# Kernel tuning notes

Measured on AMD Instinct MI355X. Metric: run time of the kernel, lower is better.

## Reference

```python
import jax, jax.numpy as jnp
import numpy as np
from jax.ops import segment_sum

N_NODES = 100000
N_EDGES = 1600000
D = 128
N_LAYERS = 4
N_GRAPHS = 512
LN_EPS = 1e-5


def setup_inputs() -> dict:
    key = jax.random.key(0)
    ks = jax.random.split(key, 8)
    x = jax.random.normal(ks[0], (N_NODES, D), dtype=jnp.float32)
    edge_index = jax.random.randint(ks[1], (2, N_EDGES), 0, N_NODES, dtype=jnp.int64)
    batch = jnp.sort(jax.random.randint(ks[2], (N_NODES,), 0, N_GRAPHS, dtype=jnp.int64))
    scale = 1.0 / np.sqrt(D)
    Ws = jax.random.normal(ks[3], (N_LAYERS, D, D), dtype=jnp.float32) * scale
    bs = jnp.zeros((N_LAYERS, D), dtype=jnp.float32)
    gammas = jnp.ones((N_LAYERS, D), dtype=jnp.float32)
    betas = jnp.zeros((N_LAYERS, D), dtype=jnp.float32)
    lin_w = jax.random.normal(ks[4], (D, 1), dtype=jnp.float32) * scale
    lin_b = jnp.zeros((1,), dtype=jnp.float32)
    return {"x": x, "edge_index": edge_index, "batch": batch, "Ws": Ws,
            "bs": bs, "gammas": gammas, "betas": betas,
            "lin_w": lin_w, "lin_b": lin_b}


def _gcn_conv(x, W, b, src, dst, deg_inv_sqrt):
    # PyG GCNConv: h = x @ W, then sym-normalized aggregation over A + I, then + bias
    h = x @ W                                   # [N, D]
    coef = deg_inv_sqrt[src] * deg_inv_sqrt[dst]  # [E]
    msg = h[src] * coef[:, None]                # [E, D] gather (memory-bound)
    agg = segment_sum(msg, dst, num_segments=x.shape[0])  # scatter-add
    agg = agg + h * (deg_inv_sqrt * deg_inv_sqrt)[:, None]  # self-loop term
    return agg + b


def _layernorm(x, gamma, beta):
    mu = jnp.mean(x, axis=-1, keepdims=True)
    var = jnp.mean(jnp.square(x - mu), axis=-1, keepdims=True)
    return (x - mu) * jax.lax.rsqrt(var + LN_EPS) * gamma + beta


def reference(x, edge_index, batch, Ws, bs, gammas, betas, lin_w, lin_b):
    n = x.shape[0]
    src, dst = edge_index[0], edge_index[1]
    # degree with self-loops (GCNConv adds self loops by default)
    deg = segment_sum(jnp.ones_like(dst, dtype=x.dtype), dst, num_segments=n) + 1.0
    deg_inv_sqrt = jax.lax.rsqrt(deg)

    h = _gcn_conv(x, Ws[0], bs[0], src, dst, deg_inv_sqrt)
    h = _layernorm(h, gammas[0], betas[0])
    h = jax.nn.relu(h)  # dropout is identity in eval mode
    for i in range(1, N_LAYERS):
        h_prev = h
        h = _gcn_conv(h, Ws[i], bs[i], src, dst, deg_inv_sqrt)
        h = _layernorm(h, gammas[i], betas[i])
        h = h + h_prev
        if i < N_LAYERS - 1:
            h = jax.nn.relu(h)

    # global mean pool over graphs
    sums = segment_sum(h, batch, num_segments=N_GRAPHS)        # [G, D]
    cnts = segment_sum(jnp.ones((n,), h.dtype), batch, num_segments=N_GRAPHS)
    pooled = sums / jnp.maximum(cnts, 1.0)[:, None]
    return pooled @ lin_w + lin_b  # [G, 1]
```

## Files before the change

kernel.cpp:

```cpp
#include <hip/hip_runtime.h>
#include <hip/hip_bf16.h>


typedef __hip_bfloat162 bf2;
typedef __attribute__((ext_vector_type(8))) short short8;
typedef __attribute__((ext_vector_type(4))) float f32x4;

__global__ __launch_bounds__(256) void k_deg(const int* __restrict__ dst,
                                             int* __restrict__ cnt, int E) {
    int base = (blockIdx.x * 256 + threadIdx.x) * 4;
    if (base + 4 <= E) {
        int4 d4 = *(const int4*)(dst + base);
        atomicAdd(&cnt[d4.x], 1);
        atomicAdd(&cnt[d4.y], 1);
        atomicAdd(&cnt[d4.z], 1);
        atomicAdd(&cnt[d4.w], 1);
    } else {
        for (int j = base; j < E; j++) atomicAdd(&cnt[dst[j]], 1);
    }
}

__global__ __launch_bounds__(256) void k_scan1(const int* __restrict__ cnt,
                                               int* __restrict__ loc,
                                               int* __restrict__ blk,
                                               float* __restrict__ dis, int n) {
    __shared__ int s[256];
    int b = blockIdx.x, tid = threadIdx.x;
    int base = b * 1024 + tid * 4;
    int v0 = (base + 0 < n) ? cnt[base + 0] : 0;
    int v1 = (base + 1 < n) ? cnt[base + 1] : 0;
    int v2 = (base + 2 < n) ? cnt[base + 2] : 0;
    int v3 = (base + 3 < n) ? cnt[base + 3] : 0;
    if (base + 0 < n) dis[base + 0] = rsqrtf((float)v0 + 1.0f);
    if (base + 1 < n) dis[base + 1] = rsqrtf((float)v1 + 1.0f);
    if (base + 2 < n) dis[base + 2] = rsqrtf((float)v2 + 1.0f);
    if (base + 3 < n) dis[base + 3] = rsqrtf((float)v3 + 1.0f);
    int tsum = v0 + v1 + v2 + v3;
    s[tid] = tsum;
    __syncthreads();
    for (int off = 1; off < 256; off <<= 1) {
        int t = (tid >= off) ? s[tid - off] : 0;
        __syncthreads();
        s[tid] += t;
        __syncthreads();
    }
    int excl = s[tid] - tsum;
    if (base + 0 < n) loc[base + 0] = excl;
    if (base + 1 < n) loc[base + 1] = excl + v0;
    if (base + 2 < n) loc[base + 2] = excl + v0 + v1;
    if (base + 3 < n) loc[base + 3] = excl + v0 + v1 + v2;
    if (tid == 255) blk[b] = s[255];
}

__global__ __launch_bounds__(128) void k_scan2(int* __restrict__ blk, int nb,
                                               int* __restrict__ total_out) {
    __shared__ int s[128];
    int tid = threadIdx.x;
    int v = (tid < nb) ? blk[tid] : 0;
    s[tid] = v;
    __syncthreads();
    for (int off = 1; off < 128; off <<= 1) {
        int t = (tid >= off) ? s[tid - off] : 0;
        __syncthreads();
        s[tid] += t;
        __syncthreads();
    }
    if (tid < nb) blk[tid] = s[tid] - v;
    if (tid == 127) *total_out = s[127];
}

__global__ void k_scan3(int* __restrict__ row_off, const int* __restrict__ blk,
                        int* __restrict__ cur, int n) {
    int d = blockIdx.x * blockDim.x + threadIdx.x;
    if (d >= n) return;
    int ro = row_off[d] + blk[d >> 10];
    row_off[d] = ro;
    cur[d] = ro;
}

__global__ __launch_bounds__(256) void k_scatter2(const int* __restrict__ src,
                                                  const int* __restrict__ dst,
                                                  int* __restrict__ cur,
                                                  const float* __restrict__ dis,
                                                  int2* __restrict__ colcf, int E) {
    int base = (blockIdx.x * 256 + threadIdx.x) * 4;
    if (base + 4 <= E) {
        int4 d4 = *(const int4*)(dst + base);
        int4 s4 = *(const int4*)(src + base);
        int dd[4] = {d4.x, d4.y, d4.z, d4.w};
        int ss[4] = {s4.x, s4.y, s4.z, s4.w};
#pragma unroll
        for (int j = 0; j < 4; j++) {
            int p = atomicAdd(&cur[dd[j]], 1);
            float cf = dis[ss[j]] * dis[dd[j]];
            colcf[p] = make_int2(ss[j], __float_as_int(cf));
        }
    } else {
        for (int j = base; j < E; j++) {
            int d = dst[j], s = src[j];
            int p = atomicAdd(&cur[d], 1);
            colcf[p] = make_int2(s, __float_as_int(dis[s] * dis[d]));
        }
    }
}

__global__ void k_prepw(const float* __restrict__ Ws, __hip_bfloat16* __restrict__ Wt) {
    int i = blockIdx.x * blockDim.x + threadIdx.x;
    int layer = i >> 14;
    int m = i & 16383;
    int j = m & 7;
    int l = (m >> 3) & 63;
    int ckb = m >> 9;
    int kb = ckb & 3;
    int c = ckb >> 2;
    int quad = l >> 4, lr = l & 15;
    int k = kb * 32 + quad * 8 + j;
    int col = c * 16 + lr;
    Wt[i] = __float2bfloat16(Ws[layer * 16384 + k * 128 + col]);
}

__global__ __launch_bounds__(256) void k_matmul(const __hip_bfloat16* __restrict__ Xb,
                                                const float* __restrict__ Xf,
                                                const __hip_bfloat16* __restrict__ Wt,
                                                __hip_bfloat16* __restrict__ Hb, int n) {
    __shared__ __align__(16) __hip_bfloat16 sX[64 * 136];
    const int tid = threadIdx.x;
    const int row0 = blockIdx.x * 64;
    if (Xf) {
        for (int i = tid; i < 2048; i += 256) {
            int r = i >> 5, c = i & 31;
            int gr = row0 + r;
            float4 v = make_float4(0.f, 0.f, 0.f, 0.f);
            if (gr < n) v = *(const float4*)(Xf + (size_t)gr * 128 + c * 4);
            union { bf2 h2[2]; uint2 u; } pk;
            pk.h2[0].x = __float2bfloat16(v.x);
            pk.h2[0].y = __float2bfloat16(v.y);
            pk.h2[1].x = __float2bfloat16(v.z);
            pk.h2[1].y = __float2bfloat16(v.w);
            *(uint2*)(sX + r * 136 + c * 4) = pk.u;
        }
    } else {
        for (int i = tid; i < 1024; i += 256) {
            int r = i >> 4, ck = i & 15;
            uint4 v = make_uint4(0, 0, 0, 0);
            int gr = row0 + r;
            if (gr < n) v = *(const uint4*)(Xb + (size_t)gr * 128 + ck * 8);
            *(uint4*)(sX + r * 136 + ck * 8) = v;
        }
    }
    __syncthreads();
    const int w = tid >> 6, l = tid & 63;
    const int quad = l >> 4, lr = l & 15;
    f32x4 acc[8];
#pragma unroll
    for (int c = 0; c < 8; c++) acc[c] = (f32x4){0.f, 0.f, 0.f, 0.f};
    short8 a[4];
#pragma unroll
    for (int kb = 0; kb < 4; kb++)
        a[kb] = *(const short8*)(sX + (w * 16 + lr) * 136 + kb * 32 + quad * 8);
#pragma unroll
    for (int c = 0; c < 8; c++) {
#pragma unroll
        for (int kb = 0; kb < 4; kb++) {
            short8 b = *(const short8*)(Wt + ((c * 4 + kb) * 64 + l) * 8);
            acc[c] = __builtin_amdgcn_mfma_f32_16x16x32_bf16(a[kb], b, acc[c], 0, 0, 0);
        }
    }
#pragma unroll
    for (int c = 0; c < 8; c++)
#pragma unroll
        for (int r = 0; r < 4; r++)
            sX[(w * 16 + quad * 4 + r) * 136 + c * 16 + lr] =
                __float2bfloat16(acc[c][r]);
#pragma unroll
    for (int p = 0; p < 4; p++) {
        int r = p * 4 + quad;
        int gr = row0 + w * 16 + r;
        uint4 v = *(const uint4*)(sX + (w * 16 + r) * 136 + lr * 8);
        if (gr < n) *(uint4*)(Hb + (size_t)gr * 128 + lr * 8) = v;
    }
}

__global__ __launch_bounds__(256) void k_node(const __hip_bfloat16* __restrict__ Hb,
                                              __hip_bfloat16* __restrict__ Xb,
                                              const int* __restrict__ row_off,
                                              const int2* __restrict__ colcf,
                                              const float* __restrict__ dis,
                                              const float* __restrict__ bias,
                                              const float* __restrict__ gamma,
                                              const float* __restrict__ beta,
                                              const float* __restrict__ lin_w,
                                              const int* __restrict__ batch,
                                              float* __restrict__ gsum,
                                              int do_relu, int do_res, int fuse_pool,
                                              int n) {
    __shared__ float spd[16];
    __shared__ int   sbt[16];
    const int wave = threadIdx.x >> 6;
    const int lane = threadIdx.x & 63;
    const int grp = lane >> 4;
    const int sub = lane & 15;
    const int node = blockIdx.x * 16 + wave * 4 + grp;
    const bool vn = node < n;
    const int nd = vn ? node : 0;
    const int e0 = vn ? row_off[node] : 0;
    const int e1 = vn ? row_off[node + 1] : 0;
    const char* hbase = (const char*)Hb;
    const unsigned suboff = (unsigned)(sub << 4);

    float dn = dis[nd];
    uint4 sv = *(const uint4*)(hbase + (((unsigned)nd) << 8) + suboff);

    float acc[8];
#pragma unroll
    for (int k = 0; k < 8; k++) acc[k] = 0.f;

    int e = e0;
    int2 p[8];
#pragma unroll
    for (int u = 0; u < 8; u++) p[u] = colcf[(e + u < e1) ? e + u : 0];

    while (__any(e < e1)) {
        uint4 v[8];
        float cf[8];
#pragma unroll
        for (int u = 0; u < 8; u++) {
            v[u] = *(const uint4*)(hbase + (((unsigned)p[u].x) << 8) + suboff);
            cf[u] = (e + u < e1) ? __int_as_float(p[u].y) : 0.f;
        }
        const int en = e + 8;
        int2 pn[8];
#pragma unroll
        for (int u = 0; u < 8; u++) pn[u] = colcf[(en + u < e1) ? en + u : 0];
#pragma unroll
        for (int u = 0; u < 8; u++) {
            float c = cf[u];
            acc[0] += __uint_as_float(v[u].x << 16) * c;
            acc[1] += __uint_as_float(v[u].x & 0xffff0000u) * c;
            acc[2] += __uint_as_float(v[u].y << 16) * c;
            acc[3] += __uint_as_float(v[u].y & 0xffff0000u) * c;
            acc[4] += __uint_as_float(v[u].z << 16) * c;
            acc[5] += __uint_as_float(v[u].z & 0xffff0000u) * c;
            acc[6] += __uint_as_float(v[u].w << 16) * c;
            acc[7] += __uint_as_float(v[u].w & 0xffff0000u) * c;
        }
#pragma unroll
        for (int u = 0; u < 8; u++) p[u] = pn[u];
        e = en;
    }

    {
        float dn2 = dn * dn;
        acc[0] += __uint_as_float(sv.x << 16) * dn2;
        acc[1] += __uint_as_float(sv.x & 0xffff0000u) * dn2;
        acc[2] += __uint_as_float(sv.y << 16) * dn2;
        acc[3] += __uint_as_float(sv.y & 0xffff0000u) * dn2;
        acc[4] += __uint_as_float(sv.z << 16) * dn2;
        acc[5] += __uint_as_float(sv.z & 0xffff0000u) * dn2;
        acc[6] += __uint_as_float(sv.w << 16) * dn2;
        acc[7] += __uint_as_float(sv.w & 0xffff0000u) * dn2;
    }
    float4 b0 = *(const float4*)(bias + sub * 8);
    float4 b1 = *(const float4*)(bias + sub * 8 + 4);
    acc[0] += b0.x; acc[1] += b0.y; acc[2] += b0.z; acc[3] += b0.w;
    acc[4] += b1.x; acc[5] += b1.y; acc[6] += b1.z; acc[7] += b1.w;

    float s = acc[0] + acc[1] + acc[2] + acc[3] + acc[4] + acc[5] + acc[6] + acc[7];
#pragma unroll
    for (int m = 8; m > 0; m >>= 1) s += __shfl_xor(s, m, 64);
    float mu = s * (1.f / 128.f);
    float vs = 0.f;
#pragma unroll
    for (int k = 0; k < 8; k++) {
        float d = acc[k] - mu;
        acc[k] = d;
        vs += d * d;
    }
#pragma unroll
    for (int m = 8; m > 0; m >>= 1) vs += __shfl_xor(vs, m, 64);
    float rs = rsqrtf(vs * (1.f / 128.f) + 1e-5f);

    float4 g0 = *(const float4*)(gamma + sub * 8);
    float4 g1 = *(const float4*)(gamma + sub * 8 + 4);
    float4 t0 = *(const float4*)(beta + sub * 8);
    float4 t1 = *(const float4*)(beta + sub * 8 + 4);
    float y[8];
    y[0] = acc[0] * rs * g0.x + t0.x;
    y[1] = acc[1] * rs * g0.y + t0.y;
    y[2] = acc[2] * rs * g0.z + t0.z;
    y[3] = acc[3] * rs * g0.w + t0.w;
    y[4] = acc[4] * rs * g1.x + t1.x;
    y[5] = acc[5] * rs * g1.y + t1.y;
    y[6] = acc[6] * rs * g1.z + t1.z;
    y[7] = acc[7] * rs * g1.w + t1.w;

    __hip_bfloat16* xp = Xb + (size_t)node * 128 + sub * 8;
    if (vn && do_res) {
        uint4 rv = *(const uint4*)xp;
        y[0] += __uint_as_float(rv.x << 16);
        y[1] += __uint_as_float(rv.x & 0xffff0000u);
        y[2] += __uint_as_float(rv.y << 16);
        y[3] += __uint_as_float(rv.y & 0xffff0000u);
        y[4] += __uint_as_float(rv.z << 16);
        y[5] += __uint_as_float(rv.z & 0xffff0000u);
        y[6] += __uint_as_float(rv.w << 16);
        y[7] += __uint_as_float(rv.w & 0xffff0000u);
    }

    if (fuse_pool) {
        float4 w0 = *(const float4*)(lin_w + sub * 8);
        float4 w1 = *(const float4*)(lin_w + sub * 8 + 4);
        float pdot = y[0] * w0.x + y[1] * w0.y + y[2] * w0.z + y[3] * w0.w +
                     y[4] * w1.x + y[5] * w1.y + y[6] * w1.z + y[7] * w1.w;
#pragma unroll
        for (int m = 8; m > 0; m >>= 1) pdot += __shfl_xor(pdot, m, 64);
        int slot = wave * 4 + grp;
        if (sub == 0) {
            spd[slot] = vn ? pdot : 0.f;
            sbt[slot] = vn ? batch[node] : -1;
        }
        __syncthreads();
        if (threadIdx.x == 0) {
            int i = 0;
            while (i < 16) {
                int b = sbt[i];
                if (b < 0) { i++; continue; }
                float acc2 = spd[i];
                int j = i + 1;
                while (j < 16 && sbt[j] == b) { acc2 += spd[j]; j++; }
                atomicAdd(&gsum[b], acc2);
                i = j;
            }
        }
    } else if (vn) {
        if (do_relu) {
#pragma unroll
            for (int k = 0; k < 8; k++) y[k] = fmaxf(y[k], 0.f);
        }
        union { bf2 h2[4]; uint4 u; } pk;
        pk.h2[0].x = __float2bfloat16(y[0]); pk.h2[0].y = __float2bfloat16(y[1]);
        pk.h2[1].x = __float2bfloat16(y[2]); pk.h2[1].y = __float2bfloat16(y[3]);
        pk.h2[2].x = __float2bfloat16(y[4]); pk.h2[2].y = __float2bfloat16(y[5]);
        pk.h2[3].x = __float2bfloat16(y[6]); pk.h2[3].y = __float2bfloat16(y[7]);
        *(uint4*)xp = pk.u;
    }
}

__global__ void k_out(const float* __restrict__ gsum, const int* __restrict__ batch,
                      const float* __restrict__ lin_b, float* __restrict__ out,
                      int n, int G) {
    int g = blockIdx.x * blockDim.x + threadIdx.x;
    if (g >= G) return;
    int lo = 0, hi = n;
    while (lo < hi) { int m = (lo + hi) >> 1; if (batch[m] < g) lo = m + 1; else hi = m; }
    int start = lo;
    hi = n;
    while (lo < hi) { int m = (lo + hi) >> 1; if (batch[m] <= g) lo = m + 1; else hi = m; }
    float c = (float)(lo - start);
    out[g] = gsum[g] / fmaxf(c, 1.f) + lin_b[0];
}

extern "C" void kernel_launch(void* const* d_in, const int* in_sizes, int n_in,
                              void* d_out, int out_size, void* d_ws, size_t ws_size,
                              hipStream_t stream) {
    const float* x      = (const float*)d_in[0];
    const int*   eidx   = (const int*)d_in[1];
    const int*   batch  = (const int*)d_in[2];
    const float* Ws     = (const float*)d_in[3];
    const float* bs     = (const float*)d_in[4];
    const float* gammas = (const float*)d_in[5];
    const float* betas  = (const float*)d_in[6];
    const float* lin_w  = (const float*)d_in[7];
    const float* lin_b  = (const float*)d_in[8];
    float* out = (float*)d_out;

    const int n = in_sizes[2];
    const int E = in_sizes[1] / 2;
    const int G = out_size;
    const int nb = (n + 1023) / 1024;

    const int* src  = eidx;
    const int* dstp = eidx + E;

    char* w = (char*)d_ws;
    size_t off = 0;
    auto alloc = [&](size_t bytes) {
        void* p = w + off;
        off = (off + bytes + 15) & ~(size_t)15;
        return p;
    };
    int*   cnt     = (int*)  alloc((size_t)n * 4);
    float* gsum    = (float*)alloc((size_t)G * 4);
    int*   row_off = (int*)  alloc((size_t)(n + 1) * 4);
    int*   blk     = (int*)  alloc(128 * 4);
    int*   cur     = (int*)  alloc((size_t)n * 4);
    float* dis     = (float*)alloc((size_t)n * 4);
    int2*  colcf   = (int2*) alloc((size_t)E * 8);
    __hip_bfloat16* hb  = (__hip_bfloat16*)alloc((size_t)n * 128 * 2);
    __hip_bfloat16* xb  = (__hip_bfloat16*)alloc((size_t)n * 128 * 2);
    __hip_bfloat16* wt  = (__hip_bfloat16*)alloc((size_t)4 * 128 * 128 * 2);
    (void)ws_size; (void)n_in;

    hipMemsetAsync(cnt, 0, (size_t)n * 4 + (size_t)G * 4, stream);
    k_deg<<<(E + 1023) / 1024, 256, 0, stream>>>(dstp, cnt, E);
    k_scan1<<<nb, 256, 0, stream>>>(cnt, row_off, blk, dis, n);
    k_scan2<<<1, 128, 0, stream>>>(blk, nb, row_off + n);
    k_scan3<<<(n + 255) / 256, 256, 0, stream>>>(row_off, blk, cur, n);
    k_scatter2<<<(E + 1023) / 1024, 256, 0, stream>>>(src, dstp, cur, dis, colcf, E);
    k_prepw<<<(4 * 128 * 128 + 255) / 256, 256, 0, stream>>>(Ws, wt);

    for (int layer = 0; layer < 4; layer++) {
        k_matmul<<<(n + 63) / 64, 256, 0, stream>>>(xb, (layer == 0) ? x : nullptr,
                                                    wt + (size_t)layer * 16384, hb, n);
        k_node<<<(n + 15) / 16, 256, 0, stream>>>(hb, xb, row_off, colcf, dis,
                                                  bs + (size_t)layer * 128,
                                                  gammas + (size_t)layer * 128,
                                                  betas + (size_t)layer * 128,
                                                  lin_w, batch, gsum,
                                                  (layer < 3) ? 1 : 0, (layer > 0) ? 1 : 0,
                                                  (layer == 3) ? 1 : 0, n);
    }
    k_out<<<(G + 255) / 256, 256, 0, stream>>>(gsum, batch, lin_b, out, n, G);
}
```

Before: 655.6 us.

## Fuse whole GCN pipeline into one persistent cooperative kernel with grid syncs

```diff
diff --git a/kernel.cpp b/kernel.cpp
--- a/kernel.cpp
+++ b/kernel.cpp
@@ -1,10 +1,14 @@
 #include <hip/hip_runtime.h>
 #include <hip/hip_bf16.h>
-
+#include <hip/hip_cooperative_groups.h>
+
+
+namespace cg = cooperative_groups;
 
 typedef __hip_bfloat162 bf2;
 typedef __attribute__((ext_vector_type(8))) short short8;
 typedef __attribute__((ext_vector_type(4))) float f32x4;
+
 
 __global__ __launch_bounds__(256) void k_deg(const int* __restrict__ dst,
                                              int* __restrict__ cnt, int E) {
@@ -360,6 +364,374 @@
     out[g] = gsum[g] / fmaxf(c, 1.f) + lin_b[0];
 }
 
+
+__global__ __launch_bounds__(256, 4) void k_all(
+    const float* __restrict__ x, const int* __restrict__ eidx,
+    const int* __restrict__ batch, const float* __restrict__ Ws,
+    const float* __restrict__ bs, const float* __restrict__ gammas,
+    const float* __restrict__ betas, const float* __restrict__ lin_w,
+    const float* __restrict__ lin_b, float* __restrict__ out,
+    int* __restrict__ cnt, int* __restrict__ row_off, int* __restrict__ blkarr,
+    int* __restrict__ cur, float* __restrict__ dis, int2* __restrict__ colcf,
+    __hip_bfloat16* __restrict__ hb, __hip_bfloat16* __restrict__ xb,
+    __hip_bfloat16* __restrict__ wt, float* __restrict__ gsum,
+    int n, int E, int G)
+{
+    cg::grid_group grid = cg::this_grid();
+    __shared__ __align__(16) char smem[64 * 136 * 2];
+    const int tid = threadIdx.x;
+    const int gid = blockIdx.x * 256 + tid;
+    const int T = gridDim.x * 256;
+    const int* src  = eidx;
+    const int* dstp = eidx + E;
+    const int nb     = (n + 1023) / 1024;
+    const int ntiles = (n + 63) / 64;
+    const int ngrp   = (n + 15) / 16;
+
+    for (int i = gid; i < n; i += T) cnt[i] = 0;
+    for (int i = gid; i < G; i += T) gsum[i] = 0.f;
+    for (int i = gid; i < 4 * 16384; i += T) {
+        int layer = i >> 14;
+        int m = i & 16383;
+        int j = m & 7, l = (m >> 3) & 63, ckb = m >> 9;
+        int kb = ckb & 3, c = ckb >> 2;
+        int quad = l >> 4, lr = l & 15;
+        int k = kb * 32 + quad * 8 + j;
+        int col = c * 16 + lr;
+        wt[i] = __float2bfloat16(Ws[layer * 16384 + k * 128 + col]);
+    }
+    grid.sync();
+
+    const int EC = (E + 3) / 4;
+    for (int idx = gid; idx < EC; idx += T) {
+        int base = idx * 4;
+        if (base + 4 <= E) {
+            int4 d4 = *(const int4*)(dstp + base);
+            atomicAdd(&cnt[d4.x], 1);
+            atomicAdd(&cnt[d4.y], 1);
+            atomicAdd(&cnt[d4.z], 1);
+            atomicAdd(&cnt[d4.w], 1);
+        } else {
+            for (int j = base; j < E; j++) atomicAdd(&cnt[dstp[j]], 1);
+        }
+    }
+    grid.sync();
+
+    {
+        int* s = (int*)smem;
+        for (int vb = blockIdx.x; vb < nb; vb += gridDim.x) {
+            int base = vb * 1024 + tid * 4;
+            int v0 = (base + 0 < n) ? cnt[base + 0] : 0;
+            int v1 = (base + 1 < n) ? cnt[base + 1] : 0;
+            int v2 = (base + 2 < n) ? cnt[base + 2] : 0;
+            int v3 = (base + 3 < n) ? cnt[base + 3] : 0;
+            if (base + 0 < n) dis[base + 0] = rsqrtf((float)v0 + 1.0f);
+            if (base + 1 < n) dis[base + 1] = rsqrtf((float)v1 + 1.0f);
+            if (base + 2 < n) dis[base + 2] = rsqrtf((float)v2 + 1.0f);
+            if (base + 3 < n) dis[base + 3] = rsqrtf((float)v3 + 1.0f);
+            int tsum = v0 + v1 + v2 + v3;
+            s[tid] = tsum;
+            __syncthreads();
+            for (int off = 1; off < 256; off <<= 1) {
+                int t = (tid >= off) ? s[tid - off] : 0;
+                __syncthreads();
+                s[tid] += t;
+                __syncthreads();
+            }
+            int excl = s[tid] - tsum;
+            if (base + 0 < n) row_off[base + 0] = excl;
+            if (base + 1 < n) row_off[base + 1] = excl + v0;
+            if (base + 2 < n) row_off[base + 2] = excl + v0 + v1;
+            if (base + 3 < n) row_off[base + 3] = excl + v0 + v1 + v2;
+            if (tid == 255) blkarr[vb] = s[255];
+            __syncthreads();
+        }
+    }
+    grid.sync();
+
+    {
+        int* s = (int*)smem;
+        int v = (tid < 128 && tid < nb) ? blkarr[tid] : 0;
+        if (tid < 128) s[tid] = v;
+        __syncthreads();
+        for (int off = 1; off < 128; off <<= 1) {
+            int t = (tid < 128 && tid >= off) ? s[tid - off] : 0;
+            __syncthreads();
+            if (tid < 128) s[tid] += t;
+            __syncthreads();
+        }
+        int total = s[127];
+        __syncthreads();
+        if (tid < 128) s[tid] -= v;
+        __syncthreads();
+        for (int d = gid; d < n; d += T) {
+            int ro = row_off[d] + s[d >> 10];
+            row_off[d] = ro;
+            cur[d] = ro;
+        }
+        if (gid == 0) row_off[n] = total;
+    }
+    grid.sync();
+
+    for (int idx = gid; idx < EC; idx += T) {
+        int base = idx * 4;
+        if (base + 4 <= E) {
+            int4 d4 = *(const int4*)(dstp + base);
+            int4 s4 = *(const int4*)(src + base);
+            int dd[4] = {d4.x, d4.y, d4.z, d4.w};
+            int ss[4] = {s4.x, s4.y, s4.z, s4.w};
+#pragma unroll
+            for (int j = 0; j < 4; j++) {
+                int p = atomicAdd(&cur[dd[j]], 1);
+                float cf = dis[ss[j]] * dis[dd[j]];
+                colcf[p] = make_int2(ss[j], __float_as_int(cf));
+            }
+        } else {
+            for (int j = base; j < E; j++) {
+                int d = dstp[j], sS = src[j];
+                int p = atomicAdd(&cur[d], 1);
+                colcf[p] = make_int2(sS, __float_as_int(dis[sS] * dis[d]));
+            }
+        }
+    }
+    grid.sync();
+
+    const int wv = tid >> 6, l = tid & 63;
+    const int quad = l >> 4, lr = l & 15;
+    for (int layer = 0; layer < 4; layer++) {
+        const __hip_bfloat16* wl = wt + layer * 16384;
+        const float* bias  = bs + layer * 128;
+        const float* gamma = gammas + layer * 128;
+        const float* beta  = betas + layer * 128;
+        const int do_relu = (layer < 3), do_res = (layer > 0), fuse_pool = (layer == 3);
+
+        {
+            __hip_bfloat16* sX = (__hip_bfloat16*)smem;
+            for (int tile = blockIdx.x; tile < ntiles; tile += gridDim.x) {
+                const int row0 = tile * 64;
+                if (layer == 0) {
+                    for (int i = tid; i < 2048; i += 256) {
+                        int r = i >> 5, c = i & 31;
+                        int gr = row0 + r;
+                        float4 v = make_float4(0.f, 0.f, 0.f, 0.f);
+                        if (gr < n) v = *(const float4*)(x + (size_t)gr * 128 + c * 4);
+                        union { bf2 h2[2]; uint2 u; } pk;
+                        pk.h2[0].x = __float2bfloat16(v.x);
+                        pk.h2[0].y = __float2bfloat16(v.y);
+                        pk.h2[1].x = __float2bfloat16(v.z);
+                        pk.h2[1].y = __float2bfloat16(v.w);
+                        *(uint2*)(sX + r * 136 + c * 4) = pk.u;
+                    }
+                } else {
+                    for (int i = tid; i < 1024; i += 256) {
+                        int r = i >> 4, ck = i & 15;
+                        uint4 v = make_uint4(0, 0, 0, 0);
+                        int gr = row0 + r;
+                        if (gr < n) v = *(const uint4*)(xb + (size_t)gr * 128 + ck * 8);
+                        *(uint4*)(sX + r * 136 + ck * 8) = v;
+                    }
+                }
+                __syncthreads();
+                f32x4 acc[8];
+#pragma unroll
+                for (int c = 0; c < 8; c++) acc[c] = (f32x4){0.f, 0.f, 0.f, 0.f};
+                short8 a[4];
+#pragma unroll
+                for (int kb = 0; kb < 4; kb++)
+                    a[kb] = *(const short8*)(sX + (wv * 16 + lr) * 136 + kb * 32 + quad * 8);
+#pragma unroll
+                for (int c = 0; c < 8; c++) {
+#pragma unroll
+                    for (int kb = 0; kb < 4; kb++) {
+                        short8 b = *(const short8*)(wl + ((c * 4 + kb) * 64 + l) * 8);
+                        acc[c] = __builtin_amdgcn_mfma_f32_16x16x32_bf16(a[kb], b, acc[c], 0, 0, 0);
+                    }
+                }
+#pragma unroll
+                for (int c = 0; c < 8; c++)
+#pragma unroll
+                    for (int r = 0; r < 4; r++)
+                        sX[(wv * 16 + quad * 4 + r) * 136 + c * 16 + lr] =
+                            __float2bfloat16(acc[c][r]);
+#pragma unroll
+                for (int p = 0; p < 4; p++) {
+                    int r = p * 4 + quad;
+                    int gr = row0 + wv * 16 + r;
+                    uint4 v = *(const uint4*)(sX + (wv * 16 + r) * 136 + lr * 8);
+                    if (gr < n) *(uint4*)(hb + (size_t)gr * 128 + lr * 8) = v;
+                }
+                __syncthreads();
+            }
+        }
+        grid.sync();
+
+        {
+            float* spd = (float*)smem;
+            int*   sbt = (int*)(smem + 64);
+            const int grp = l >> 4, sub = l & 15;
+            const char* hbase = (const char*)hb;
+            const unsigned suboff = (unsigned)(sub << 4);
+            for (int vb = blockIdx.x; vb < ngrp; vb += gridDim.x) {
+                const int node = vb * 16 + wv * 4 + grp;
+                const bool vn = node < n;
+                const int nd = vn ? node : 0;
+                const int e0 = vn ? row_off[node] : 0;
+                const int e1 = vn ? row_off[node + 1] : 0;
+
+                float dn = dis[nd];
+                uint4 sv = *(const uint4*)(hbase + (((unsigned)nd) << 8) + suboff);
+
+                float acc[8];
+#pragma unroll
+                for (int k = 0; k < 8; k++) acc[k] = 0.f;
+
+                int e = e0;
+                int2 p[8];
+#pragma unroll
+                for (int u = 0; u < 8; u++) p[u] = colcf[(e + u < e1) ? e + u : 0];
+
+                while (__any(e < e1)) {
+                    uint4 v[8];
+                    float cf[8];
+#pragma unroll
+                    for (int u = 0; u < 8; u++) {
+                        v[u] = *(const uint4*)(hbase + (((unsigned)p[u].x) << 8) + suboff);
+                        cf[u] = (e + u < e1) ? __int_as_float(p[u].y) : 0.f;
+                    }
+                    const int en = e + 8;
+                    int2 pn[8];
+#pragma unroll
+                    for (int u = 0; u < 8; u++) pn[u] = colcf[(en + u < e1) ? en + u : 0];
+#pragma unroll
+                    for (int u = 0; u < 8; u++) {
+                        float c = cf[u];
+                        acc[0] += __uint_as_float(v[u].x << 16) * c;
+                        acc[1] += __uint_as_float(v[u].x & 0xffff0000u) * c;
+                        acc[2] += __uint_as_float(v[u].y << 16) * c;
+                        acc[3] += __uint_as_float(v[u].y & 0xffff0000u) * c;
+                        acc[4] += __uint_as_float(v[u].z << 16) * c;
+                        acc[5] += __uint_as_float(v[u].z & 0xffff0000u) * c;
+                        acc[6] += __uint_as_float(v[u].w << 16) * c;
+                        acc[7] += __uint_as_float(v[u].w & 0xffff0000u) * c;
+                    }
+#pragma unroll
+                    for (int u = 0; u < 8; u++) p[u] = pn[u];
+                    e = en;
+                }
+
+                {
+                    float dn2 = dn * dn;
+                    acc[0] += __uint_as_float(sv.x << 16) * dn2;
+                    acc[1] += __uint_as_float(sv.x & 0xffff0000u) * dn2;
+                    acc[2] += __uint_as_float(sv.y << 16) * dn2;
+                    acc[3] += __uint_as_float(sv.y & 0xffff0000u) * dn2;
+                    acc[4] += __uint_as_float(sv.z << 16) * dn2;
+                    acc[5] += __uint_as_float(sv.z & 0xffff0000u) * dn2;
+                    acc[6] += __uint_as_float(sv.w << 16) * dn2;
+                    acc[7] += __uint_as_float(sv.w & 0xffff0000u) * dn2;
+                }
+                float4 b0 = *(const float4*)(bias + sub * 8);
+                float4 b1 = *(const float4*)(bias + sub * 8 + 4);
+                acc[0] += b0.x; acc[1] += b0.y; acc[2] += b0.z; acc[3] += b0.w;
+                acc[4] += b1.x; acc[5] += b1.y; acc[6] += b1.z; acc[7] += b1.w;
+
+                float s = acc[0] + acc[1] + acc[2] + acc[3] + acc[4] + acc[5] + acc[6] + acc[7];
+#pragma unroll
+                for (int m = 8; m > 0; m >>= 1) s += __shfl_xor(s, m, 64);
+                float mu = s * (1.f / 128.f);
+                float vs = 0.f;
+#pragma unroll
+                for (int k = 0; k < 8; k++) {
+                    float d = acc[k] - mu;
+                    acc[k] = d;
+                    vs += d * d;
+                }
+#pragma unroll
+                for (int m = 8; m > 0; m >>= 1) vs += __shfl_xor(vs, m, 64);
+                float rs = rsqrtf(vs * (1.f / 128.f) + 1e-5f);
+
+                float4 g0 = *(const float4*)(gamma + sub * 8);
+                float4 g1 = *(const float4*)(gamma + sub * 8 + 4);
+                float4 t0 = *(const float4*)(beta + sub * 8);
+                float4 t1 = *(const float4*)(beta + sub * 8 + 4);
+                float y[8];
+                y[0] = acc[0] * rs * g0.x + t0.x;
+                y[1] = acc[1] * rs * g0.y + t0.y;
+                y[2] = acc[2] * rs * g0.z + t0.z;
+                y[3] = acc[3] * rs * g0.w + t0.w;
+                y[4] = acc[4] * rs * g1.x + t1.x;
+                y[5] = acc[5] * rs * g1.y + t1.y;
+                y[6] = acc[6] * rs * g1.z + t1.z;
+                y[7] = acc[7] * rs * g1.w + t1.w;
+
+                __hip_bfloat16* xp = xb + (size_t)node * 128 + sub * 8;
+                if (vn && do_res) {
+                    uint4 rv = *(const uint4*)xp;
+                    y[0] += __uint_as_float(rv.x << 16);
+                    y[1] += __uint_as_float(rv.x & 0xffff0000u);
+                    y[2] += __uint_as_float(rv.y << 16);
+                    y[3] += __uint_as_float(rv.y & 0xffff0000u);
+                    y[4] += __uint_as_float(rv.z << 16);
+                    y[5] += __uint_as_float(rv.z & 0xffff0000u);
+                    y[6] += __uint_as_float(rv.w << 16);
+                    y[7] += __uint_as_float(rv.w & 0xffff0000u);
+                }
+
+                if (fuse_pool) {
+                    float4 w0 = *(const float4*)(lin_w + sub * 8);
+                    float4 w1 = *(const float4*)(lin_w + sub * 8 + 4);
+                    float pdot = y[0] * w0.x + y[1] * w0.y + y[2] * w0.z + y[3] * w0.w +
+                                 y[4] * w1.x + y[5] * w1.y + y[6] * w1.z + y[7] * w1.w;
+#pragma unroll
+                    for (int m = 8; m > 0; m >>= 1) pdot += __shfl_xor(pdot, m, 64);
+                    int slot = wv * 4 + grp;
+                    if (sub == 0) {
+                        spd[slot] = vn ? pdot : 0.f;
+                        sbt[slot] = vn ? batch[node] : -1;
+                    }
+                    __syncthreads();
+                    if (tid == 0) {
+                        int i = 0;
+                        while (i < 16) {
+                            int b = sbt[i];
+                            if (b < 0) { i++; continue; }
+                            float acc2 = spd[i];
+                            int j = i + 1;
+                            while (j < 16 && sbt[j] == b) { acc2 += spd[j]; j++; }
+                            atomicAdd(&gsum[b], acc2);
+                            i = j;
+                        }
+                    }
+                    __syncthreads();
+                } else if (vn) {
+                    if (do_relu) {
+#pragma unroll
+                        for (int k = 0; k < 8; k++) y[k] = fmaxf(y[k], 0.f);
+                    }
+                    union { bf2 h2[4]; uint4 u; } pk;
+                    pk.h2[0].x = __float2bfloat16(y[0]); pk.h2[0].y = __float2bfloat16(y[1]);
+                    pk.h2[1].x = __float2bfloat16(y[2]); pk.h2[1].y = __float2bfloat16(y[3]);
+                    pk.h2[2].x = __float2bfloat16(y[4]); pk.h2[2].y = __float2bfloat16(y[5]);
+                    pk.h2[3].x = __float2bfloat16(y[6]); pk.h2[3].y = __float2bfloat16(y[7]);
+                    *(uint4*)xp = pk.u;
+                }
+            }
+        }
+        grid.sync();
+    }
+
+    for (int g = gid; g < G; g += T) {
+        int lo = 0, hi = n;
+        while (lo < hi) { int m = (lo + hi) >> 1; if (batch[m] < g) lo = m + 1; else hi = m; }
+        int start = lo;
+        hi = n;
+        while (lo < hi) { int m = (lo + hi) >> 1; if (batch[m] <= g) lo = m + 1; else hi = m; }
+        float c = (float)(lo - start);
+        out[g] = gsum[g] / fmaxf(c, 1.f) + lin_b[0];
+    }
+}
+
+
 extern "C" void kernel_launch(void* const* d_in, const int* in_sizes, int n_in,
                               void* d_out, int out_size, void* d_ws, size_t ws_size,
                               hipStream_t stream) {
@@ -374,9 +746,9 @@
     const float* lin_b  = (const float*)d_in[8];
     float* out = (float*)d_out;
 
-    const int n = in_sizes[2];
-    const int E = in_sizes[1] / 2;
-    const int G = out_size;
+    int n = in_sizes[2];
+    int E = in_sizes[1] / 2;
+    int G = out_size;
     const int nb = (n + 1023) / 1024;
 
     const int* src  = eidx;
@@ -392,7 +764,7 @@
     int*   cnt     = (int*)  alloc((size_t)n * 4);
     float* gsum    = (float*)alloc((size_t)G * 4);
     int*   row_off = (int*)  alloc((size_t)(n + 1) * 4);
-    int*   blk     = (int*)  alloc(128 * 4);
+    int*   blkarr  = (int*)  alloc(128 * 4);
     int*   cur     = (int*)  alloc((size_t)n * 4);
     float* dis     = (float*)alloc((size_t)n * 4);
     int2*  colcf   = (int2*) alloc((size_t)E * 8);
@@ -401,24 +773,41 @@
     __hip_bfloat16* wt  = (__hip_bfloat16*)alloc((size_t)4 * 128 * 128 * 2);
     (void)ws_size; (void)n_in;
 
-    hipMemsetAsync(cnt, 0, (size_t)n * 4 + (size_t)G * 4, stream);
-    k_deg<<<(E + 1023) / 1024, 256, 0, stream>>>(dstp, cnt, E);
-    k_scan1<<<nb, 256, 0, stream>>>(cnt, row_off, blk, dis, n);
-    k_scan2<<<1, 128, 0, stream>>>(blk, nb, row_off + n);
-    k_scan3<<<(n + 255) / 256, 256, 0, stream>>>(row_off, blk, cur, n);
-    k_scatter2<<<(E + 1023) / 1024, 256, 0, stream>>>(src, dstp, cur, dis, colcf, E);
-    k_prepw<<<(4 * 128 * 128 + 255) / 256, 256, 0, stream>>>(Ws, wt);
-
-    for (int layer = 0; layer < 4; layer++) {
-        k_matmul<<<(n + 63) / 64, 256, 0, stream>>>(xb, (layer == 0) ? x : nullptr,
-                                                    wt + (size_t)layer * 16384, hb, n);
-        k_node<<<(n + 15) / 16, 256, 0, stream>>>(hb, xb, row_off, colcf, dis,
-                                                  bs + (size_t)layer * 128,
-                                                  gammas + (size_t)layer * 128,
-                                                  betas + (size_t)layer * 128,
-                                                  lin_w, batch, gsum,
-                                                  (layer < 3) ? 1 : 0, (layer > 0) ? 1 : 0,
-                                                  (layer == 3) ? 1 : 0, n);
-    }
-    k_out<<<(G + 255) / 256, 256, 0, stream>>>(gsum, batch, lin_b, out, n, G);
-}
+    bool coop_ok = false;
+    int maxPerCU = 0;
+    hipError_t qerr = hipOccupancyMaxActiveBlocksPerMultiprocessor(
+        &maxPerCU, reinterpret_cast<const void*>(k_all), 256, 0);
+    if (qerr == hipSuccess && maxPerCU >= 3) {
+        int nblk = maxPerCU * 256;
+        if (nblk > 1024) nblk = 1024;
+        void* args[] = { &x, &eidx, &batch, &Ws, &bs, &gammas, &betas, &lin_w,
+                         &lin_b, &out, &cnt, &row_off, &blkarr, &cur, &dis,
+                         &colcf, &hb, &xb, &wt, &gsum, &n, &E, &G };
+        hipError_t lerr = hipLaunchCooperativeKernel((const void*)k_all,
+                                                     dim3(nblk), dim3(256),
+                                                     args, 0, stream);
+        coop_ok = (lerr == hipSuccess);
+    }
+
+    if (!coop_ok) {
+        hipMemsetAsync(cnt, 0, (size_t)n * 4 + (size_t)G * 4, stream);
+        k_deg<<<(E + 1023) / 1024, 256, 0, stream>>>(dstp, cnt, E);
+        k_scan1<<<nb, 256, 0, stream>>>(cnt, row_off, blkarr, dis, n);
+        k_scan2<<<1, 128, 0, stream>>>(blkarr, nb, row_off + n);
+        k_scan3<<<(n + 255) / 256, 256, 0, stream>>>(row_off, blkarr, cur, n);
+        k_scatter2<<<(E + 1023) / 1024, 256, 0, stream>>>(src, dstp, cur, dis, colcf, E);
+        k_prepw<<<(4 * 128 * 128 + 255) / 256, 256, 0, stream>>>(Ws, wt);
+        for (int layer = 0; layer < 4; layer++) {
+            k_matmul<<<(n + 63) / 64, 256, 0, stream>>>(xb, (layer == 0) ? x : nullptr,
+                                                        wt + (size_t)layer * 16384, hb, n);
+            k_node<<<(n + 15) / 16, 256, 0, stream>>>(hb, xb, row_off, colcf, dis,
+                                                      bs + (size_t)layer * 128,
+                                                      gammas + (size_t)layer * 128,
+                                                      betas + (size_t)layer * 128,
+                                                      lin_w, batch, gsum,
+                                                      (layer < 3) ? 1 : 0, (layer > 0) ? 1 : 0,
+                                                      (layer == 3) ? 1 : 0, n);
+        }
+        k_out<<<(G + 255) / 256, 256, 0, stream>>>(gsum, batch, lin_b, out, n, G);
+    }
+}
```

Measured after the change: 667.5 us. No clear change (+1.8%).

## Fuse next layer's matmul into node aggregation kernel with ping-pong H buffers

Applied to the files above, without the earlier changes.

```diff
diff --git a/kernel.cpp b/kernel.cpp
--- a/kernel.cpp
+++ b/kernel.cpp
@@ -119,34 +119,23 @@
     Wt[i] = __float2bfloat16(Ws[layer * 16384 + k * 128 + col]);
 }
 
-__global__ __launch_bounds__(256) void k_matmul(const __hip_bfloat16* __restrict__ Xb,
-                                                const float* __restrict__ Xf,
+__global__ __launch_bounds__(256) void k_matmul(const float* __restrict__ Xf,
                                                 const __hip_bfloat16* __restrict__ Wt,
                                                 __hip_bfloat16* __restrict__ Hb, int n) {
     __shared__ __align__(16) __hip_bfloat16 sX[64 * 136];
     const int tid = threadIdx.x;
     const int row0 = blockIdx.x * 64;
-    if (Xf) {
-        for (int i = tid; i < 2048; i += 256) {
-            int r = i >> 5, c = i & 31;
-            int gr = row0 + r;
-            float4 v = make_float4(0.f, 0.f, 0.f, 0.f);
-            if (gr < n) v = *(const float4*)(Xf + (size_t)gr * 128 + c * 4);
-            union { bf2 h2[2]; uint2 u; } pk;
-            pk.h2[0].x = __float2bfloat16(v.x);
-            pk.h2[0].y = __float2bfloat16(v.y);
-            pk.h2[1].x = __float2bfloat16(v.z);
-            pk.h2[1].y = __float2bfloat16(v.w);
-            *(uint2*)(sX + r * 136 + c * 4) = pk.u;
-        }
-    } else {
-        for (int i = tid; i < 1024; i += 256) {
-            int r = i >> 4, ck = i & 15;
-            uint4 v = make_uint4(0, 0, 0, 0);
-            int gr = row0 + r;
-            if (gr < n) v = *(const uint4*)(Xb + (size_t)gr * 128 + ck * 8);
-            *(uint4*)(sX + r * 136 + ck * 8) = v;
-        }
+    for (int i = tid; i < 2048; i += 256) {
+        int r = i >> 5, c = i & 31;
+        int gr = row0 + r;
+        float4 v = make_float4(0.f, 0.f, 0.f, 0.f);
+        if (gr < n) v = *(const float4*)(Xf + (size_t)gr * 128 + c * 4);
+        union { bf2 h2[2]; uint2 u; } pk;
+        pk.h2[0].x = __float2bfloat16(v.x);
+        pk.h2[0].y = __float2bfloat16(v.y);
+        pk.h2[1].x = __float2bfloat16(v.z);
+        pk.h2[1].y = __float2bfloat16(v.w);
+        *(uint2*)(sX + r * 136 + c * 4) = pk.u;
     }
     __syncthreads();
     const int w = tid >> 6, l = tid & 63;
@@ -181,31 +170,36 @@
     }
 }
 
-__global__ __launch_bounds__(256) void k_node(const __hip_bfloat16* __restrict__ Hb,
-                                              __hip_bfloat16* __restrict__ Xb,
-                                              const int* __restrict__ row_off,
-                                              const int2* __restrict__ colcf,
-                                              const float* __restrict__ dis,
-                                              const float* __restrict__ bias,
-                                              const float* __restrict__ gamma,
-                                              const float* __restrict__ beta,
-                                              const float* __restrict__ lin_w,
-                                              const int* __restrict__ batch,
-                                              float* __restrict__ gsum,
-                                              int do_relu, int do_res, int fuse_pool,
-                                              int n) {
+__global__ __launch_bounds__(256) void k_nodeF(const __hip_bfloat16* __restrict__ Hin,
+                                               __hip_bfloat16* __restrict__ Hout,
+                                               __hip_bfloat16* __restrict__ Xb,
+                                               const int* __restrict__ row_off,
+                                               const int2* __restrict__ colcf,
+                                               const float* __restrict__ dis,
+                                               const float* __restrict__ bias,
+                                               const float* __restrict__ gamma,
+                                               const float* __restrict__ beta,
+                                               const __hip_bfloat16* __restrict__ wnext,
+                                               const float* __restrict__ lin_w,
+                                               const int* __restrict__ batch,
+                                               float* __restrict__ gsum,
+                                               int do_relu, int do_res, int do_mm,
+                                               int fuse_pool, int n) {
+    __shared__ __align__(16) __hip_bfloat16 sY[16 * 136];
+    __shared__ __align__(16) __hip_bfloat16 sH[16 * 136];
     __shared__ float spd[16];
     __shared__ int   sbt[16];
-    const int wave = threadIdx.x >> 6;
-    const int lane = threadIdx.x & 63;
+    const int tid = threadIdx.x;
+    const int wv = tid >> 6;
+    const int lane = tid & 63;
     const int grp = lane >> 4;
     const int sub = lane & 15;
-    const int node = blockIdx.x * 16 + wave * 4 + grp;
+    const int node = blockIdx.x * 16 + wv * 4 + grp;
     const bool vn = node < n;
     const int nd = vn ? node : 0;
     const int e0 = vn ? row_off[node] : 0;
     const int e1 = vn ? row_off[node + 1] : 0;
-    const char* hbase = (const char*)Hb;
+    const char* hbase = (const char*)Hin;
     const unsigned suboff = (unsigned)(sub << 4);
 
     float dn = dis[nd];
@@ -306,6 +300,16 @@
         y[6] += __uint_as_float(rv.w << 16);
         y[7] += __uint_as_float(rv.w & 0xffff0000u);
     }
+    if (do_relu) {
+#pragma unroll
+        for (int k = 0; k < 8; k++) y[k] = fmaxf(y[k], 0.f);
+    }
+
+    union { bf2 h2[4]; uint4 u; } pk;
+    pk.h2[0].x = __float2bfloat16(y[0]); pk.h2[0].y = __float2bfloat16(y[1]);
+    pk.h2[1].x = __float2bfloat16(y[2]); pk.h2[1].y = __float2bfloat16(y[3]);
+    pk.h2[2].x = __float2bfloat16(y[4]); pk.h2[2].y = __float2bfloat16(y[5]);
+    pk.h2[3].x = __float2bfloat16(y[6]); pk.h2[3].y = __float2bfloat16(y[7]);
 
     if (fuse_pool) {
         float4 w0 = *(const float4*)(lin_w + sub * 8);
@@ -314,13 +318,13 @@
                      y[4] * w1.x + y[5] * w1.y + y[6] * w1.z + y[7] * w1.w;
 #pragma unroll
         for (int m = 8; m > 0; m >>= 1) pdot += __shfl_xor(pdot, m, 64);
-        int slot = wave * 4 + grp;
+        int slot = wv * 4 + grp;
         if (sub == 0) {
             spd[slot] = vn ? pdot : 0.f;
             sbt[slot] = vn ? batch[node] : -1;
         }
         __syncthreads();
-        if (threadIdx.x == 0) {
+        if (tid == 0) {
             int i = 0;
             while (i < 16) {
                 int b = sbt[i];
@@ -332,17 +336,45 @@
                 i = j;
             }
         }
-    } else if (vn) {
-        if (do_relu) {
-#pragma unroll
-            for (int k = 0; k < 8; k++) y[k] = fmaxf(y[k], 0.f);
-        }
-        union { bf2 h2[4]; uint4 u; } pk;
-        pk.h2[0].x = __float2bfloat16(y[0]); pk.h2[0].y = __float2bfloat16(y[1]);
-        pk.h2[1].x = __float2bfloat16(y[2]); pk.h2[1].y = __float2bfloat16(y[3]);
-        pk.h2[2].x = __float2bfloat16(y[4]); pk.h2[2].y = __float2bfloat16(y[5]);
-        pk.h2[3].x = __float2bfloat16(y[6]); pk.h2[3].y = __float2bfloat16(y[7]);
-        *(uint4*)xp = pk.u;
+        return;
+    }
+
+    if (vn) *(uint4*)xp = pk.u;
+
+    if (do_mm) {
+        uint4 zero = make_uint4(0, 0, 0, 0);
+        *(uint4*)(sY + (wv * 4 + grp) * 136 + sub * 8) = vn ? pk.u : zero;
+        __syncthreads();
+        short8 a[4];
+#pragma unroll
+        for (int kb = 0; kb < 4; kb++)
+            a[kb] = *(const short8*)(sY + sub * 136 + kb * 32 + grp * 8);
+        f32x4 hacc[2];
+#pragma unroll
+        for (int ci = 0; ci < 2; ci++) hacc[ci] = (f32x4){0.f, 0.f, 0.f, 0.f};
+#pragma unroll
+        for (int ci = 0; ci < 2; ci++) {
+            const int c = wv * 2 + ci;
+#pragma unroll
+            for (int kb = 0; kb < 4; kb++) {
+                short8 b = *(const short8*)(wnext + ((c * 4 + kb) * 64 + lane) * 8);
+                hacc[ci] = __builtin_amdgcn_mfma_f32_16x16x32_bf16(a[kb], b, hacc[ci], 0, 0, 0);
+            }
+        }
+#pragma unroll
+        for (int ci = 0; ci < 2; ci++) {
+            const int c = wv * 2 + ci;
+#pragma unroll
+            for (int r = 0; r < 4; r++)
+                sH[(grp * 4 + r) * 136 + c * 16 + sub] = __float2bfloat16(hacc[ci][r]);
+        }
+        __syncthreads();
+        int row = tid >> 4, ck = tid & 15;
+        int gr = blockIdx.x * 16 + row;
+        if (gr < n) {
+            uint4 v = *(const uint4*)(sH + row * 136 + ck * 8);
+            *(uint4*)(Hout + (size_t)gr * 128 + ck * 8) = v;
+        }
     }
 }
 
@@ -392,33 +424,40 @@
     int*   cnt     = (int*)  alloc((size_t)n * 4);
     float* gsum    = (float*)alloc((size_t)G * 4);
     int*   row_off = (int*)  alloc((size_t)(n + 1) * 4);
-    int*   blk     = (int*)  alloc(128 * 4);
+    int*   blkarr  = (int*)  alloc(128 * 4);
     int*   cur     = (int*)  alloc((size_t)n * 4);
     float* dis     = (float*)alloc((size_t)n * 4);
     int2*  colcf   = (int2*) alloc((size_t)E * 8);
-    __hip_bfloat16* hb  = (__hip_bfloat16*)alloc((size_t)n * 128 * 2);
+    __hip_bfloat16* hbA = (__hip_bfloat16*)alloc((size_t)n * 128 * 2);
+    __hip_bfloat16* hbB = (__hip_bfloat16*)alloc((size_t)n * 128 * 2);
     __hip_bfloat16* xb  = (__hip_bfloat16*)alloc((size_t)n * 128 * 2);
     __hip_bfloat16* wt  = (__hip_bfloat16*)alloc((size_t)4 * 128 * 128 * 2);
     (void)ws_size; (void)n_in;
 
     hipMemsetAsync(cnt, 0, (size_t)n * 4 + (size_t)G * 4, stream);
     k_deg<<<(E + 1023) / 1024, 256, 0, stream>>>(dstp, cnt, E);
-    k_scan1<<<nb, 256, 0, stream>>>(cnt, row_off, blk, dis, n);
-    k_scan2<<<1, 128, 0, stream>>>(blk, nb, row_off + n);
-    k_scan3<<<(n + 255) / 256, 256, 0, stream>>>(row_off, blk, cur, n);
+    k_scan1<<<nb, 256, 0, stream>>>(cnt, row_off, blkarr, dis, n);
+    k_scan2<<<1, 128, 0, stream>>>(blkarr, nb, row_off + n);
+    k_scan3<<<(n + 255) / 256, 256, 0, stream>>>(row_off, blkarr, cur, n);
     k_scatter2<<<(E + 1023) / 1024, 256, 0, stream>>>(src, dstp, cur, dis, colcf, E);
     k_prepw<<<(4 * 128 * 128 + 255) / 256, 256, 0, stream>>>(Ws, wt);
 
+    k_matmul<<<(n + 63) / 64, 256, 0, stream>>>(x, wt, hbA, n);
+
+    __hip_bfloat16* hin  = hbA;
+    __hip_bfloat16* hout = hbB;
     for (int layer = 0; layer < 4; layer++) {
-        k_matmul<<<(n + 63) / 64, 256, 0, stream>>>(xb, (layer == 0) ? x : nullptr,
-                                                    wt + (size_t)layer * 16384, hb, n);
-        k_node<<<(n + 15) / 16, 256, 0, stream>>>(hb, xb, row_off, colcf, dis,
-                                                  bs + (size_t)layer * 128,
-                                                  gammas + (size_t)layer * 128,
-                                                  betas + (size_t)layer * 128,
-                                                  lin_w, batch, gsum,
-                                                  (layer < 3) ? 1 : 0, (layer > 0) ? 1 : 0,
-                                                  (layer == 3) ? 1 : 0, n);
+        const int do_mm = (layer < 3);
+        k_nodeF<<<(n + 15) / 16, 256, 0, stream>>>(
+            hin, hout, xb, row_off, colcf, dis,
+            bs + (size_t)layer * 128,
+            gammas + (size_t)layer * 128,
+            betas + (size_t)layer * 128,
+            wt + (size_t)(do_mm ? (layer + 1) : 0) * 16384,
+            lin_w, batch, gsum,
+            (layer < 3) ? 1 : 0, (layer > 0) ? 1 : 0, do_mm,
+            (layer == 3) ? 1 : 0, n);
+        __hip_bfloat16* t = hin; hin = hout; hout = t;
     }
     k_out<<<(G + 255) / 256, 256, 0, stream>>>(gsum, batch, lin_b, out, n, G);
 }
```

After: 679.8 us. 3.7% more time.
